# Kernel optimization log

Measured on AMD Instinct MI355X. Metric: run time of the kernel, lower is better.

The kernel has to match this reference:

```python
import jax, jax.numpy as jnp
import numpy as np

NV, NR = 30000, 1000
EVV, EVI, EIV = 400000, 120000, 120000
VD, RD, ED = 16, 8, 2
HID, OUT, H1 = 64, 64, 2


def _seg_softmax(logits, seg, n):
    # numerically stable segment softmax over destination nodes
    m = jax.ops.segment_max(logits, seg, num_segments=n)
    m = jnp.where(jnp.isfinite(m), m, 0.0)
    ex = jnp.exp(logits - m[seg])
    den = jax.ops.segment_sum(ex, seg, num_segments=n)
    return ex / (den[seg] + 1e-16)


def _gatv2(x_src, x_dst, src, dst, ea, Wl, Wr, We, att, b, heads, n_dst, concat):
    # PyG GATv2Conv: e = att . leaky_relu(Wl x_j + Wr x_i + We e_ij); out = sum_j softmax(e) * Wl x_j
    C = att.shape[-1]
    hl = (x_src @ Wl).reshape(-1, heads, C)
    hr = (x_dst @ Wr).reshape(-1, heads, C)
    he = (ea @ We).reshape(-1, heads, C)
    xj = hl[src]                                   # [E, H, C]
    g = jax.nn.leaky_relu(xj + hr[dst] + he, 0.2)
    logits = jnp.einsum('ehc,hc->eh', g, att)      # [E, H]
    alpha = _seg_softmax(logits, dst, n_dst)
    out = jax.ops.segment_sum(xj * alpha[..., None], dst, num_segments=n_dst)
    out = out.reshape(n_dst, heads * C) if concat else out.mean(axis=1)
    return out + b


def _self_loops(src, dst, ea, n):
    # PyG add_self_loops(fill_value='mean'): self-loop edge_attr = per-dst mean of incoming edge_attr
    deg = jax.ops.segment_sum(jnp.ones((ea.shape[0],), ea.dtype), dst, num_segments=n)
    mean = jax.ops.segment_sum(ea, dst, num_segments=n) / jnp.maximum(deg, 1.0)[:, None]
    ar = jnp.arange(n, dtype=src.dtype)
    return jnp.concatenate([src, ar]), jnp.concatenate([dst, ar]), jnp.concatenate([ea, mean], axis=0)


def _ln(x, g, b):
    m = x.mean(-1, keepdims=True)
    v = ((x - m) ** 2).mean(-1, keepdims=True)
    return (x - m) * jax.lax.rsqrt(v + 1e-5) * g + b


def setup_inputs() -> dict:
    key = jax.random.key(0)
    ks = iter(jax.random.split(key, 80))
    def rn(shape, s=1.0):
        return jax.random.normal(next(ks), shape, jnp.float32) * s
    def ri(n, hi):
        return jax.random.randint(next(ks), (n,), 0, hi, jnp.int32)
    d = {'x_veh': rn((NV, VD)), 'x_rsu': rn((NR, RD)),
         'ea_v2v': rn((EVV, ED)), 'ea_v2i': rn((EVI, ED)), 'ea_i2v': rn((EIV, ED)),
         'src_v2v': ri(EVV, NV), 'dst_v2v': ri(EVV, NV),
         'src_v2i': ri(EVI, NV), 'dst_v2i': ri(EVI, NR),
         'src_i2v': ri(EIV, NR), 'dst_i2v': ri(EIV, NV)}
    H1C = H1 * HID
    for rel, di_s, di_d in (('vv', VD, VD), ('vi', VD, RD), ('iv', RD, VD)):
        d['Wl_' + rel + '1'] = rn((di_s, H1C), 0.1)
        d['Wr_' + rel + '1'] = rn((di_d, H1C), 0.1)
        d['We_' + rel + '1'] = rn((ED, H1C), 0.1)
        d['att_' + rel + '1'] = rn((H1, HID), 0.1)
        d['b_' + rel + '1'] = jnp.zeros((H1C,), jnp.float32)
    for rel in ('vv', 'vi', 'iv'):
        d['Wl_' + rel + '2'] = rn((H1C, OUT), 0.1)
        d['Wr_' + rel + '2'] = rn((H1C, OUT), 0.1)
        d['We_' + rel + '2'] = rn((ED, OUT), 0.1)
        d['att_' + rel + '2'] = rn((1, OUT), 0.1)
        d['b_' + rel + '2'] = jnp.zeros((OUT,), jnp.float32)
    d['ln_vg'] = jnp.ones((OUT,), jnp.float32)
    d['ln_vb'] = jnp.zeros((OUT,), jnp.float32)
    d['ln_rg'] = jnp.ones((OUT,), jnp.float32)
    d['ln_rb'] = jnp.zeros((OUT,), jnp.float32)
    return d


def reference(x_veh, x_rsu, ea_v2v, ea_v2i, ea_i2v,
              src_v2v, dst_v2v, src_v2i, dst_v2i, src_i2v, dst_i2v,
              Wl_vv1, Wr_vv1, We_vv1, att_vv1, b_vv1,
              Wl_vi1, Wr_vi1, We_vi1, att_vi1, b_vi1,
              Wl_iv1, Wr_iv1, We_iv1, att_iv1, b_iv1,
              Wl_vv2, Wr_vv2, We_vv2, att_vv2, b_vv2,
              Wl_vi2, Wr_vi2, We_vi2, att_vi2, b_vi2,
              Wl_iv2, Wr_iv2, We_iv2, att_iv2, b_iv2,
              ln_vg, ln_vb, ln_rg, ln_rb):
    s_vv, d_vv, ea_vv = _self_loops(src_v2v, dst_v2v, ea_v2v, NV)
    # layer 1 (heads=2, concat=True), HeteroConv aggr='sum'
    v1 = (_gatv2(x_veh, x_veh, s_vv, d_vv, ea_vv, Wl_vv1, Wr_vv1, We_vv1, att_vv1, b_vv1, H1, NV, True)
          + _gatv2(x_rsu, x_veh, src_i2v, dst_i2v, ea_i2v, Wl_iv1, Wr_iv1, We_iv1, att_iv1, b_iv1, H1, NV, True))
    r1 = _gatv2(x_veh, x_rsu, src_v2i, dst_v2i, ea_v2i, Wl_vi1, Wr_vi1, We_vi1, att_vi1, b_vi1, H1, NR, True)
    v1 = jax.nn.elu(v1)
    r1 = jax.nn.elu(r1)
    # layer 2 (heads=1, concat=False -> mean over 1 head)
    v2 = (_gatv2(v1, v1, s_vv, d_vv, ea_vv, Wl_vv2, Wr_vv2, We_vv2, att_vv2, b_vv2, 1, NV, False)
          + _gatv2(r1, v1, src_i2v, dst_i2v, ea_i2v, Wl_iv2, Wr_iv2, We_iv2, att_iv2, b_iv2, 1, NV, False))
    r2 = _gatv2(v1, r1, src_v2i, dst_v2i, ea_v2i, Wl_vi2, Wr_vi2, We_vi2, att_vi2, b_vi2, 1, NR, False)
    return jnp.concatenate([_ln(v2, ln_vg, ln_vb), _ln(r2, ln_rg, ln_rb)], axis=0)
```

## Files before the change

kernel.cpp:

```cpp
#include <hip/hip_runtime.h>
#include <hip/hip_fp16.h>

constexpr int NV = 30000, NR = 1000;
constexpr int EVV = 400000, EVI = 120000, EIV = 120000;
constexpr int ETOT = EVV + EIV + EVI;
constexpr int VB = (NV + 3) / 4;
constexpr float LOFF = 4.0f;

struct __align__(8) Edge { int s; __half2 ea; };
struct __align__(16) TRec { int s; int d; __half2 ea; int r; };
typedef __half2 h2;

__device__ __forceinline__ h2 h2shfl_xor(h2 v, int m) {
  int i = *(int*)&v;
  i = __shfl_xor(i, m);
  return *(h2*)&i;
}
__device__ __forceinline__ h2 h2max(h2 a, h2 b) {
  h2 r;
  asm("v_pk_max_f16 %0, %1, %2" : "=v"(r) : "v"(a), "v"(b));
  return r;
}

constexpr size_t OFF_CUR_VV = 0;
constexpr size_t OFF_CUR_IV = OFF_CUR_VV + NV;
constexpr size_t OFF_CUR_VI = OFF_CUR_IV + NV;
constexpr size_t ZERO_END   = OFF_CUR_VI + NR;
constexpr size_t OFF_PTR_VV = ZERO_END;
constexpr size_t OFF_PTR_IV = OFF_PTR_VV + NV + 2;
constexpr size_t OFF_PTR_VI = OFF_PTR_IV + NV + 2;
constexpr size_t OFF_E_VV   = (OFF_PTR_VI + NR + 2 + 3) & ~(size_t)3;
constexpr size_t OFF_E_IV   = OFF_E_VV + (size_t)EVV * 2;
constexpr size_t OFF_E_VI   = OFF_E_IV + (size_t)EIV * 2;
constexpr size_t OFF_TMP    = (OFF_E_VI + (size_t)EVI * 2 + 3) & ~(size_t)3;
constexpr size_t OFF_H      = (OFF_TMP + (size_t)ETOT * 4 + 3) & ~(size_t)3;
constexpr size_t OFF_HL_VV1 = OFF_H;
constexpr size_t OFF_HR_VV1 = OFF_HL_VV1 + (size_t)NV * 64;
constexpr size_t OFF_HR_IV1 = OFF_HR_VV1 + (size_t)NV * 64;
constexpr size_t OFF_HL_VI1 = OFF_HR_IV1 + (size_t)NV * 64;
// ... 142 lines not shown
  for (int i = tid; i < ROWS * K / 2; i += 64 * NW) {
    int gi = r0 * (K / 2) + i;
    float2 f = (gi < n * (K / 2)) ? __half22float2(X2[gi]) : make_float2(0.f, 0.f);
    ((float*)xs)[2 * i] = f.x;
    ((float*)xs)[2 * i + 1] = f.y;
  }
  __syncthreads();
  int lane = tid & 63, wv = tid >> 6;
  const float* __restrict__ W = wv == 0 ? W0 : wv == 1 ? W1 : wv == 2 ? W2 : W3;
  __half* __restrict__ Y = wv == 0 ? Y0 : wv == 1 ? Y1 : wv == 2 ? Y2 : Y3;
  float acc[ROWS];
#pragma unroll
  for (int r = 0; r < ROWS; r++) acc[r] = 0.f;
  for (int k4 = 0; k4 < K / 4; k4++) {
    float w0 = W[(4 * k4 + 0) * 64 + lane];
    float w1 = W[(4 * k4 + 1) * 64 + lane];
    float w2 = W[(4 * k4 + 2) * 64 + lane];
    float w3 = W[(4 * k4 + 3) * 64 + lane];
#pragma unroll
    for (int r = 0; r < ROWS; r++) {
      float4 x4 = *(const float4*)&xs[r][4 * k4];
      acc[r] = fmaf(x4.x, w0, acc[r]);
      acc[r] = fmaf(x4.y, w1, acc[r]);
      acc[r] = fmaf(x4.z, w2, acc[r]);
      acc[r] = fmaf(x4.w, w3, acc[r]);
    }
  }
#pragma unroll
  for (int r = 0; r < ROWS; r++)
    if (r0 + r < n) Y[(size_t)(r0 + r) * 64 + lane] = __float2half(acc[r]);
}


template<bool SELF>
__device__ __forceinline__ void gatW2(int d, int lane, int eg, int cg,
    int b, int cnt, int es0, int eab0,
    const Edge* __restrict__ ed,
    const __half* __restrict__ hl, float4 hrr,
    const float* __restrict__ We, const float* __restrict__ att,
    float* acc, float& den0, float& den1) {
  h2 hrc2[4], av2[4], w02[4], w12[4];
  const h2* hrp = (const h2*)&hrr;
#pragma unroll
  for (int j = 0; j < 4; j++) hrc2[j] = hrp[j];
#pragma unroll
  for (int j = 0; j < 4; j++) {
    int c = cg * 4 + j;
    av2[j] = __floats2half2_rn(att[c], att[64 + c]);
    w02[j] = __floats2half2_rn(We[c], We[64 + c]);
    w12[j] = __floats2half2_rn(We[128 + c], We[192 + c]);
  }
  const h2 c02 = __float2half2_rn(0.2f);
  h2 acc2[4];
#pragma unroll
  for (int j = 0; j < 4; j++) acc2[j] = __float2half2_rn(0.f);
  float sum0 = 0.f, sum1 = 0.f;
  auto proc = [&](float4 r, int eab, bool v) {
    const h2* hp = (const h2*)&r;
    h2 eh = *(h2*)&eab;
    h2 ef0 = __low2half2(eh), ef1 = __high2half2(eh);
    h2 lacc = __float2half2_rn(0.f);
#pragma unroll
    for (int j = 0; j < 4; j++) {
      h2 g = __hfma2(ef0, w02[j], __hadd2(hp[j], hrc2[j]));
      g = __hfma2(ef1, w12[j], g);
      h2 lr = h2max(g, __hmul2(c02, g));
      lacc = __hfma2(lr, av2[j], lacc);
    }
#pragma unroll
    for (int o = 1; o <= 8; o <<= 1) lacc = __hadd2(lacc, h2shfl_xor(lacc, o));
    float2 lf = __half22float2(lacc);
    float ex0 = v ? __expf(lf.x - LOFF) : 0.f;
    float ex1 = v ? __expf(lf.y - LOFF) : 0.f;
    h2 exh = __floats2half2_rn(ex0, ex1);
#pragma unroll
    for (int j = 0; j < 4; j++) acc2[j] = __hfma2(exh, hp[j], acc2[j]);
    den0 += ex0; den1 += ex1;
  };
  auto doWin = [&](int es, int eab, int wlen) {
    int kk = 0;
    for (; kk + 16 <= wlen; kk += 16) {
      int k0 = kk + eg, k1 = kk + 4 + eg, k2 = kk + 8 + eg, k3 = kk + 12 + eg;
      int s0 = __shfl(es, k0), ea0 = __shfl(eab, k0);
      int s1 = __shfl(es, k1), ea1 = __shfl(eab, k1);
      int s2 = __shfl(es, k2), ea2 = __shfl(eab, k2);
      int s3 = __shfl(es, k3), ea3 = __shfl(eab, k3);
      float4 r0 = *(const float4*)&hl[(size_t)s0 * 128 + cg * 8];
      float4 r1 = *(const float4*)&hl[(size_t)s1 * 128 + cg * 8];
      float4 r2 = *(const float4*)&hl[(size_t)s2 * 128 + cg * 8];
      float4 r3 = *(const float4*)&hl[(size_t)s3 * 128 + cg * 8];
      proc(r0, ea0, true);
      proc(r1, ea1, true);
      proc(r2, ea2, true);
      proc(r3, ea3, true);
    }
    for (; kk < wlen; kk += 4) {
      int k0 = kk + eg;
      int s0 = __shfl(es, k0), ea0 = __shfl(eab, k0);
      float4 r0 = *(const float4*)&hl[(size_t)s0 * 128 + cg * 8];
      proc(r0, ea0, k0 < wlen);
    }
  };
  if (SELF) {
    float2 f = __half22float2(*(h2*)&eab0);
    sum0 += f.x; sum1 += f.y;
  }
  doWin(es0, eab0, min(64, cnt));
  for (int wf = 64; wf < cnt; wf += 64) {
    int idx = wf + lane;
    int es = 0, eab = 0;
    if (idx < cnt) { Edge e = ed[b + idx]; es = e.s; eab = *(const int*)&e.ea; }
    if (SELF) {
      float2 f = __half22float2(*(h2*)&eab);
      sum0 += f.x; sum1 += f.y;
    }
    doWin(es, eab, min(64, cnt - wf));
  }
  if (SELF) {
#pragma unroll
    for (int o = 1; o <= 32; o <<= 1) { sum0 += __shfl_xor(sum0, o); sum1 += __shfl_xor(sum1, o); }
    float dg = fmaxf((float)cnt, 1.f);
    __half2 mh = __floats2half2_rn(sum0 / dg, sum1 / dg);
    int meab = *(const int*)&mh;
    float4 rS = *(const float4*)&hl[(size_t)d * 128 + cg * 8];
    proc(rS, meab, eg == 0);
  }
#pragma unroll
  for (int o = 16; o <= 32; o <<= 1) {
#pragma unroll
    for (int j = 0; j < 4; j++) acc2[j] = __hadd2(acc2[j], h2shfl_xor(acc2[j], o));
    den0 += __shfl_xor(den0, o);
    den1 += __shfl_xor(den1, o);
  }
#pragma unroll
  for (int j = 0; j < 4; j++) {
    float2 f = __half22float2(acc2[j]);
    acc[2 * j] = f.x; acc[2 * j + 1] = f.y;
  }
}

template<bool SELF>
__device__ __forceinline__ void gatW1(int d, int lane, int eg8, int cg8,
    int b, int cnt, int es0, int eab0,
    const Edge* __restrict__ ed,
    const __half* __restrict__ hl, float4 hrr,
    const float* __restrict__ We, const float* __restrict__ att,
    float* acc, float& den) {
  h2 hrc2[4], av2[4], w02[4], w12[4];
  const h2* hrp = (const h2*)&hrr;
#pragma unroll
  for (int j = 0; j < 4; j++) hrc2[j] = hrp[j];
#pragma unroll
  for (int j = 0; j < 4; j++) {
    int c = cg8 * 8 + 2 * j;
    av2[j] = __floats2half2_rn(att[c], att[c + 1]);
    w02[j] = __floats2half2_rn(We[c], We[c + 1]);
    w12[j] = __floats2half2_rn(We[64 + c], We[64 + c + 1]);
  }
  const h2 c02 = __float2half2_rn(0.2f);
  h2 acc2[4];
#pragma unroll
  for (int j = 0; j < 4; j++) acc2[j] = __float2half2_rn(0.f);
  float sum0 = 0.f, sum1 = 0.f;
  auto proc = [&](float4 r, int eab, bool v) {
    const h2* hp = (const h2*)&r;
    h2 eh = *(h2*)&eab;
    h2 ef0 = __low2half2(eh), ef1 = __high2half2(eh);
    h2 lacc = __float2half2_rn(0.f);
#pragma unroll
    for (int j = 0; j < 4; j++) {
      h2 g = __hfma2(ef0, w02[j], __hadd2(hp[j], hrc2[j]));
      g = __hfma2(ef1, w12[j], g);
      h2 lr = h2max(g, __hmul2(c02, g));
      lacc = __hfma2(lr, av2[j], lacc);
    }
#pragma unroll
    for (int o = 1; o <= 4; o <<= 1) lacc = __hadd2(lacc, h2shfl_xor(lacc, o));
    float2 lf = __half22float2(lacc);
    float ex = v ? __expf(lf.x + lf.y - LOFF) : 0.f;
    h2 exh = __float2half2_rn(ex);
#pragma unroll
    for (int j = 0; j < 4; j++) acc2[j] = __hfma2(exh, hp[j], acc2[j]);
    den += ex;
  };
  auto doWin = [&](int es, int eab, int wlen) {
    int kk = 0;
    for (; kk + 32 <= wlen; kk += 32) {
      int k0 = kk + eg8, k1 = kk + 8 + eg8, k2 = kk + 16 + eg8, k3 = kk + 24 + eg8;
      int s0 = __shfl(es, k0), ea0 = __shfl(eab, k0);
      int s1 = __shfl(es, k1), ea1 = __shfl(eab, k1);
      int s2 = __shfl(es, k2), ea2 = __shfl(eab, k2);
      int s3 = __shfl(es, k3), ea3 = __shfl(eab, k3);
      float4 r0 = *(const float4*)&hl[(size_t)s0 * 64 + cg8 * 8];
      float4 r1 = *(const float4*)&hl[(size_t)s1 * 64 + cg8 * 8];
      float4 r2 = *(const float4*)&hl[(size_t)s2 * 64 + cg8 * 8];
      float4 r3 = *(const float4*)&hl[(size_t)s3 * 64 + cg8 * 8];
      proc(r0, ea0, true);
      proc(r1, ea1, true);
      proc(r2, ea2, true);
      proc(r3, ea3, true);
    }
    for (; kk < wlen; kk += 8) {
      int k0 = kk + eg8;
      int s0 = __shfl(es, k0), ea0 = __shfl(eab, k0);
      float4 r0 = *(const float4*)&hl[(size_t)s0 * 64 + cg8 * 8];
      proc(r0, ea0, k0 < wlen);
    }
  };
  if (SELF) {
    float2 f = __half22float2(*(h2*)&eab0);
    sum0 += f.x; sum1 += f.y;
  }
  doWin(es0, eab0, min(64, cnt));
  for (int wf = 64; wf < cnt; wf += 64) {
    int idx = wf + lane;
    int es = 0, eab = 0;
    if (idx < cnt) { Edge e = ed[b + idx]; es = e.s; eab = *(const int*)&e.ea; }
    if (SELF) {
      float2 f = __half22float2(*(h2*)&eab);
      sum0 += f.x; sum1 += f.y;
    }
    doWin(es, eab, min(64, cnt - wf));
  }
  if (SELF) {
#pragma unroll
    for (int o = 1; o <= 32; o <<= 1) { sum0 += __shfl_xor(sum0, o); sum1 += __shfl_xor(sum1, o); }
    float dg = fmaxf((float)cnt, 1.f);
    __half2 mh = __floats2half2_rn(sum0 / dg, sum1 / dg);
    int meab = *(const int*)&mh;
    float4 rS = *(const float4*)&hl[(size_t)d * 64 + cg8 * 8];
    proc(rS, meab, eg8 == 0);
  }
#pragma unroll
  for (int o = 8; o <= 32; o <<= 1) {
#pragma unroll
    for (int j = 0; j < 4; j++) acc2[j] = __hadd2(acc2[j], h2shfl_xor(acc2[j], o));
    den += __shfl_xor(den, o);
  }
#pragma unroll
  for (int j = 0; j < 4; j++) {
    float2 f = __half22float2(acc2[j]);
    acc[2 * j] = f.x; acc[2 * j + 1] = f.y;
  }
}

__global__ __launch_bounds__(256) void k_gat_l1(
    const int* ptr_vv, const Edge* e_vv,
    const __half* hl_vv, const __half* hr_vv, const float* We_vv, const float* att_vv,
    const int* ptr_iv, const Edge* e_iv,
    const __half* hl_iv, const __half* hr_iv, const float* We_iv, const float* att_iv,
    const int* ptr_vi, const Edge* e_vi,
    const __half* hl_vi, const __half* hr_vi, const float* We_vi, const float* att_vi,
    const float* b_vv, const float* b_iv, const float* b_vi,
    __half* __restrict__ v1, __half* __restrict__ r1) {
  __shared__ float sm[4][16][10];
  int lane = threadIdx.x & 63, wv = threadIdx.x >> 6;
  int eg = lane >> 4, cg = lane & 15;
  if (blockIdx.x >= NR) {
    int w = (blockIdx.x - NR) * 4 + wv;
    if (w >= NV) return;
    int b1 = ptr_vv[w], c1 = ptr_vv[w + 1] - b1;
    int b2 = ptr_iv[w], c2 = ptr_iv[w + 1] - b2;
    int es1 = 0, ea1 = 0, es2 = 0, ea2 = 0;
    if (lane < c1) { Edge e = e_vv[b1 + lane]; es1 = e.s; ea1 = *(const int*)&e.ea; }
    if (lane < c2) { Edge e = e_iv[b2 + lane]; es2 = e.s; ea2 = *(const int*)&e.ea; }
    float4 hrv = *(const float4*)&hr_vv[(size_t)w * 128 + cg * 8];
    float4 hri = *(const float4*)&hr_iv[(size_t)w * 128 + cg * 8];
    float acc[8];
    float d0 = 0.f, d1 = 0.f, oc[8];
    gatW2<true>(w, lane, eg, cg, b1, c1, es1, ea1, e_vv, hl_vv, hrv, We_vv, att_vv, acc, d0, d1);
#pragma unroll
    for (int j = 0; j < 8; j++) oc[j] = acc[j] / (((j & 1) ? d1 : d0) + 1e-16f);
    d0 = d1 = 0.f;
    gatW2<false>(w, lane, eg, cg, b2, c2, es2, ea2, e_iv, hl_iv, hri, We_iv, att_iv, acc, d0, d1);
#pragma unroll
    for (int j = 0; j < 8; j++) oc[j] += acc[j] / (((j & 1) ? d1 : d0) + 1e-16f);
    if (eg == 0) {
      float x[8];
#pragma unroll
      for (int j = 0; j < 8; j++) {
        int c = cg * 4 + (j >> 1);
        int idx = (j & 1) * 64 + c;
        float v = oc[j] + b_vv[idx] + b_iv[idx];
        x[j] = v > 0.f ? v : __expf(v) - 1.f;
      }
      __half2 h0a = __floats2half2_rn(x[0], x[2]), h0b = __floats2half2_rn(x[4], x[6]);
      __half2 h1a = __floats2half2_rn(x[1], x[3]), h1b = __floats2half2_rn(x[5], x[7]);
      float2 p0, p1;
      ((__half2*)&p0)[0] = h0a; ((__half2*)&p0)[1] = h0b;
      ((__half2*)&p1)[0] = h1a; ((__half2*)&p1)[1] = h1b;
      *(float2*)&v1[(size_t)w * 128 + cg * 4]      = p0;
      *(float2*)&v1[(size_t)w * 128 + 64 + cg * 4] = p1;
    }
  } else {
    int dd = blockIdx.x;
    int bfull = ptr_vi[dd], cntf = ptr_vi[dd + 1] - bfull;
    int q = (cntf + 3) >> 2;
    int off = min(wv * q, cntf);
    int cnt = min(q, cntf - off);
    int b = bfull + off;
    int es0 = 0, ea0 = 0;
    if (lane < cnt) { Edge e = e_vi[b + lane]; es0 = e.s; ea0 = *(const int*)&e.ea; }
    float4 hrr = *(const float4*)&hr_vi[(size_t)dd * 128 + cg * 8];
    float acc[8];
    float d0 = 0.f, d1 = 0.f;
    gatW2<false>(dd, lane, eg, cg, b, cnt, es0, ea0, e_vi, hl_vi, hrr, We_vi, att_vi, acc, d0, d1);
    if (eg == 0) {
#pragma unroll
      for (int j = 0; j < 8; j++) sm[wv][cg][j] = acc[j];
      sm[wv][cg][8] = d0; sm[wv][cg][9] = d1;
    }
    __syncthreads();
    if (wv == 0) {
#pragma unroll
      for (int j = 0; j < 8; j++)
        acc[j] = sm[0][cg][j] + sm[1][cg][j] + sm[2][cg][j] + sm[3][cg][j];
      d0 = sm[0][cg][8] + sm[1][cg][8] + sm[2][cg][8] + sm[3][cg][8];
      d1 = sm[0][cg][9] + sm[1][cg][9] + sm[2][cg][9] + sm[3][cg][9];
      if (eg == 0) {
        float x[8];
#pragma unroll
        for (int j = 0; j < 8; j++) {
          int c = cg * 4 + (j >> 1);
          int idx = (j & 1) * 64 + c;
          float v = acc[j] / (((j & 1) ? d1 : d0) + 1e-16f) + b_vi[idx];
          x[j] = v > 0.f ? v : __expf(v) - 1.f;
        }
        __half2 h0a = __floats2half2_rn(x[0], x[2]), h0b = __floats2half2_rn(x[4], x[6]);
        __half2 h1a = __floats2half2_rn(x[1], x[3]), h1b = __floats2half2_rn(x[5], x[7]);
        float2 p0, p1;
        ((__half2*)&p0)[0] = h0a; ((__half2*)&p0)[1] = h0b;
        ((__half2*)&p1)[0] = h1a; ((__half2*)&p1)[1] = h1b;
        *(float2*)&r1[(size_t)dd * 128 + cg * 4]      = p0;
        *(float2*)&r1[(size_t)dd * 128 + 64 + cg * 4] = p1;
      }
    }
  }
}

__global__ __launch_bounds__(256) void k_gat_l2(
    const int* ptr_vv, const Edge* e_vv,
    const __half* hl_vv, const __half* hr_vv, const float* We_vv, const float* att_vv,
    const int* ptr_iv, const Edge* e_iv,
    const __half* hl_iv, const __half* hr_iv, const float* We_iv, const float* att_iv,
    const int* ptr_vi, const Edge* e_vi,
    const __half* hl_vi, const __half* hr_vi, const float* We_vi, const float* att_vi,
    const float* b_vv, const float* b_iv, const float* b_vi,
    const float* ln_vg, const float* ln_vb, const float* ln_rg, const float* ln_rb,
    float* __restrict__ out) {
  __shared__ float sm[4][8][9];
  int lane = threadIdx.x & 63, wv = threadIdx.x >> 6;
  int eg8 = lane >> 3, cg8 = lane & 7;
  if (blockIdx.x >= NR) {
    int w = (blockIdx.x - NR) * 4 + wv;
    if (w >= NV) return;
    int b1 = ptr_vv[w], c1 = ptr_vv[w + 1] - b1;
    int b2 = ptr_iv[w], c2 = ptr_iv[w + 1] - b2;
    int es1 = 0, ea1 = 0, es2 = 0, ea2 = 0;
    if (lane < c1) { Edge e = e_vv[b1 + lane]; es1 = e.s; ea1 = *(const int*)&e.ea; }
    if (lane < c2) { Edge e = e_iv[b2 + lane]; es2 = e.s; ea2 = *(const int*)&e.ea; }
    float4 hrv = *(const float4*)&hr_vv[(size_t)w * 64 + cg8 * 8];
    float4 hri = *(const float4*)&hr_iv[(size_t)w * 64 + cg8 * 8];
    float acc[8];
    float dn = 0.f, oc[8];
    gatW1<true>(w, lane, eg8, cg8, b1, c1, es1, ea1, e_vv, hl_vv, hrv, We_vv, att_vv, acc, dn);
#pragma unroll
    for (int j = 0; j < 8; j++) oc[j] = acc[j] / (dn + 1e-16f);
    dn = 0.f;
    gatW1<false>(w, lane, eg8, cg8, b2, c2, es2, ea2, e_iv, hl_iv, hri, We_iv, att_iv, acc, dn);
    float x[8], s = 0.f;
#pragma unroll
    for (int j = 0; j < 8; j++) {
      int c = cg8 * 8 + j;
      x[j] = oc[j] + acc[j] / (dn + 1e-16f) + b_vv[c] + b_iv[c];
      s += x[j];
    }
#pragma unroll
    for (int o = 1; o <= 4; o <<= 1) s += __shfl_xor(s, o);
    float mu = s * (1.f / 64.f);
    float v = 0.f;
#pragma unroll
    for (int j = 0; j < 8; j++) { float dx = x[j] - mu; v = fmaf(dx, dx, v); }
#pragma unroll
    for (int o = 1; o <= 4; o <<= 1) v += __shfl_xor(v, o);
    float rstd = rsqrtf(v * (1.f / 64.f) + 1e-5f);
    if (eg8 == 0) {
      float4 o0, o1;
      float* ov = (float*)&o0;
#pragma unroll
      for (int j = 0; j < 4; j++) {
        int c = cg8 * 8 + j;
        ov[j] = (x[j] - mu) * rstd * ln_vg[c] + ln_vb[c];
      }
      ov = (float*)&o1;
#pragma unroll
      for (int j = 0; j < 4; j++) {
        int c = cg8 * 8 + 4 + j;
        ov[j] = (x[4 + j] - mu) * rstd * ln_vg[c] + ln_vb[c];
      }
      *(float4*)&out[(size_t)w * 64 + cg8 * 8]     = o0;
      *(float4*)&out[(size_t)w * 64 + cg8 * 8 + 4] = o1;
    }
  } else {
    int dd = blockIdx.x;
    int bfull = ptr_vi[dd], cntf = ptr_vi[dd + 1] - bfull;
    int q = (cntf + 3) >> 2;
    int off = min(wv * q, cntf);
    int cnt = min(q, cntf - off);
    int b = bfull + off;
    int es0 = 0, ea0 = 0;
    if (lane < cnt) { Edge e = e_vi[b + lane]; es0 = e.s; ea0 = *(const int*)&e.ea; }
    float4 hrr = *(const float4*)&hr_vi[(size_t)dd * 64 + cg8 * 8];
    float acc[8];
    float dn = 0.f;
    gatW1<false>(dd, lane, eg8, cg8, b, cnt, es0, ea0, e_vi, hl_vi, hrr, We_vi, att_vi, acc, dn);
    if (eg8 == 0) {
#pragma unroll
      for (int j = 0; j < 8; j++) sm[wv][cg8][j] = acc[j];
      sm[wv][cg8][8] = dn;
    }
    __syncthreads();
    if (wv == 0) {
#pragma unroll
      for (int j = 0; j < 8; j++)
        acc[j] = sm[0][cg8][j] + sm[1][cg8][j] + sm[2][cg8][j] + sm[3][cg8][j];
      dn = sm[0][cg8][8] + sm[1][cg8][8] + sm[2][cg8][8] + sm[3][cg8][8];
      float x[8], s = 0.f;
#pragma unroll
      for (int j = 0; j < 8; j++) {
        int c = cg8 * 8 + j;
        x[j] = acc[j] / (dn + 1e-16f) + b_vi[c];
        s += x[j];
      }
#pragma unroll
      for (int o = 1; o <= 4; o <<= 1) s += __shfl_xor(s, o);
      float mu = s * (1.f / 64.f);
      float v = 0.f;
#pragma unroll
      for (int j = 0; j < 8; j++) { float dx = x[j] - mu; v = fmaf(dx, dx, v); }
#pragma unroll
      for (int o = 1; o <= 4; o <<= 1) v += __shfl_xor(v, o);
      float rstd = rsqrtf(v * (1.f / 64.f) + 1e-5f);
      if (eg8 == 0) {
#pragma unroll
        for (int j = 0; j < 8; j++) {
          int c = cg8 * 8 + j;
          out[(size_t)(NV + dd) * 64 + c] = (x[j] - mu) * rstd * ln_rg[c] + ln_rb[c];
        }
      }
    }
  }
}

extern "C" void kernel_launch(void* const* d_in, const int* in_sizes, int n_in,
                              void* d_out, int out_size, void* d_ws, size_t ws_size,
                              hipStream_t stream) {
  const float* x_veh  = (const float*)d_in[0];
  const float* x_rsu  = (const float*)d_in[1];
  const float* ea_vv  = (const float*)d_in[2];
// ... 53 lines not shown
  Edge* e_iv = (Edge*)(ws + OFF_E_IV);
  Edge* e_vi = (Edge*)(ws + OFF_E_VI);
  TRec* tmp  = (TRec*)(ws + OFF_TMP);

  __half* hl_vv1 = (__half*)(ws + OFF_HL_VV1);
  __half* hr_vv1 = (__half*)(ws + OFF_HR_VV1);
  __half* hr_iv1 = (__half*)(ws + OFF_HR_IV1);
  __half* hl_vi1 = (__half*)(ws + OFF_HL_VI1);
  __half* hl_iv1 = (__half*)(ws + OFF_HL_IV1);
  __half* hr_vi1 = (__half*)(ws + OFF_HR_VI1);
  __half* v1 = (__half*)(ws + OFF_V1);
  __half* r1 = (__half*)(ws + OFF_R1);
  __half* hl_vv2 = (__half*)(ws + OFF_HL_VV2);
  __half* hr_vv2 = (__half*)(ws + OFF_HR_VV2);
  __half* hr_iv2 = (__half*)(ws + OFF_HR_IV2);
  __half* hl_vi2 = (__half*)(ws + OFF_HL_VI2);
  __half* hl_iv2 = (__half*)(ws + OFF_HL_IV2);
  __half* hr_vi2 = (__half*)(ws + OFF_HR_VI2);

  (void)hipMemsetAsync(ws, 0, ZERO_END * sizeof(float), stream);

  k_build1<<<(ETOT + 255) / 256, 256, 0, stream>>>(
      src_vv, dst_vv, ea_vv, src_iv, dst_iv, ea_iv, src_vi, dst_vi, ea_vi,
      cur_vv, cur_iv, cur_vi, tmp);
  k_scan3<<<3, 1024, 0, stream>>>(cur_vv, ptr_vv, NV, cur_iv, ptr_iv, NV, cur_vi, ptr_vi, NR);
  k_build2<<<(ETOT + 255) / 256, 256, 0, stream>>>(tmp, ptr_vv, ptr_iv, ptr_vi,
      e_vv, e_iv, e_vi);

  k_gemm1<16, 4><<<(NV + 7) / 8, 256, 0, stream>>>(x_veh,
      Wl_vv1, Wr_vv1, Wr_iv1, Wl_vi1, hl_vv1, hr_vv1, hr_iv1, hl_vi1, NV);
  k_gemm1<8, 2><<<(NR + 7) / 8, 256, 0, stream>>>(x_rsu,
      Wl_iv1, Wr_vi1, nullptr, nullptr, hl_iv1, hr_vi1, nullptr, nullptr, NR);

  k_gat_l1<<<NR + VB, 256, 0, stream>>>(
      ptr_vv, e_vv, hl_vv1, hr_vv1, We_vv1, att_vv1,
      ptr_iv, e_iv, hl_iv1, hr_iv1, We_iv1, att_iv1,
      ptr_vi, e_vi, hl_vi1, hr_vi1, We_vi1, att_vi1,
      b_vv1, b_iv1, b_vi1, v1, r1);

  k_gemm2<4><<<(NV + 15) / 16, 256, 0, stream>>>(v1,
      Wl_vv2, Wr_vv2, Wr_iv2, Wl_vi2, hl_vv2, hr_vv2, hr_iv2, hl_vi2, NV);
  k_gemm2<2><<<(NR + 15) / 16, 128, 0, stream>>>(r1,
      Wl_iv2, Wr_vi2, nullptr, nullptr, hl_iv2, hr_vi2, nullptr, nullptr, NR);

  k_gat_l2<<<NR + VB, 256, 0, stream>>>(
      ptr_vv, e_vv, hl_vv2, hr_vv2, We_vv2, att_vv2,
      ptr_iv, e_iv, hl_iv2, hr_iv2, We_iv2, att_iv2,
      ptr_vi, e_vi, hl_vi2, hr_vi2, We_vi2, att_vi2,
      b_vv2, b_iv2, b_vi2, ln_vg, ln_vb, ln_rg, ln_rb, out);
  (void)in_sizes; (void)n_in; (void)out_size; (void)ws_size;
}
```

Baseline: 317.6 us.

## Split each vehicle node's edge work across two wavefronts with LDS combine

Each vehicle destination node is now handled by two wavefronts instead of one. One takes the first half of the v2v edges, the other takes the remaining v2v edges plus all i2v edges. Partial numerators, denominators and edge-attribute sums are combined through shared memory after a barrier, and the self-loop term is then applied by the first wavefront. This aims to cut per-node serial latency and balance uneven degrees, at the cost of doubling the vehicle block count, adding a block-wide barrier, and leaving the second wavefront idle during the epilogue.

```diff
diff --git a/kernel.cpp b/kernel.cpp
--- a/kernel.cpp
+++ b/kernel.cpp
@@ -4,7 +4,7 @@
 constexpr int NV = 30000, NR = 1000;
 constexpr int EVV = 400000, EVI = 120000, EIV = 120000;
 constexpr int ETOT = EVV + EIV + EVI;
-constexpr int VB = (NV + 3) / 4;
+constexpr int VB2 = NV / 2;
 constexpr float LOFF = 4.0f;
 
 struct __align__(8) Edge { int s; __half2 ea; };
@@ -213,13 +213,12 @@
 }
 
 
-template<bool SELF>
-__device__ __forceinline__ void gatW2(int d, int lane, int eg, int cg,
+__device__ __forceinline__ void gatP2(int lane, int eg, int cg,
     int b, int cnt, int es0, int eab0,
     const Edge* __restrict__ ed,
     const __half* __restrict__ hl, float4 hrr,
     const float* __restrict__ We, const float* __restrict__ att,
-    float* acc, float& den0, float& den1) {
+    float* acc, float& den0, float& den1, float& sum0, float& sum1) {
   h2 hrc2[4], av2[4], w02[4], w12[4];
   const h2* hrp = (const h2*)&hrr;
 #pragma unroll
@@ -235,7 +234,7 @@
   h2 acc2[4];
 #pragma unroll
   for (int j = 0; j < 4; j++) acc2[j] = __float2half2_rn(0.f);
-  float sum0 = 0.f, sum1 = 0.f;
+  den0 = den1 = 0.f; sum0 = 0.f; sum1 = 0.f;
   auto proc = [&](float4 r, int eab, bool v) {
     const h2* hp = (const h2*)&r;
     h2 eh = *(h2*)&eab;
@@ -282,7 +281,7 @@
       proc(r0, ea0, k0 < wlen);
     }
   };
-  if (SELF) {
+  {
     float2 f = __half22float2(*(h2*)&eab0);
     sum0 += f.x; sum1 += f.y;
   }
@@ -291,20 +290,9 @@
     int idx = wf + lane;
     int es = 0, eab = 0;
     if (idx < cnt) { Edge e = ed[b + idx]; es = e.s; eab = *(const int*)&e.ea; }
-    if (SELF) {
-      float2 f = __half22float2(*(h2*)&eab);
-      sum0 += f.x; sum1 += f.y;
-    }
+    float2 f = __half22float2(*(h2*)&eab);
+    sum0 += f.x; sum1 += f.y;
     doWin(es, eab, min(64, cnt - wf));
-  }
-  if (SELF) {
-#pragma unroll
-    for (int o = 1; o <= 32; o <<= 1) { sum0 += __shfl_xor(sum0, o); sum1 += __shfl_xor(sum1, o); }
-    float dg = fmaxf((float)cnt, 1.f);
-    __half2 mh = __floats2half2_rn(sum0 / dg, sum1 / dg);
-    int meab = *(const int*)&mh;
-    float4 rS = *(const float4*)&hl[(size_t)d * 128 + cg * 8];
-    proc(rS, meab, eg == 0);
   }
 #pragma unroll
   for (int o = 16; o <= 32; o <<= 1) {
@@ -314,19 +302,20 @@
     den1 += __shfl_xor(den1, o);
   }
 #pragma unroll
+  for (int o = 1; o <= 32; o <<= 1) { sum0 += __shfl_xor(sum0, o); sum1 += __shfl_xor(sum1, o); }
+#pragma unroll
   for (int j = 0; j < 4; j++) {
     float2 f = __half22float2(acc2[j]);
     acc[2 * j] = f.x; acc[2 * j + 1] = f.y;
   }
 }
 
-template<bool SELF>
-__device__ __forceinline__ void gatW1(int d, int lane, int eg8, int cg8,
+__device__ __forceinline__ void gatP1(int lane, int eg8, int cg8,
     int b, int cnt, int es0, int eab0,
     const Edge* __restrict__ ed,
     const __half* __restrict__ hl, float4 hrr,
     const float* __restrict__ We, const float* __restrict__ att,
-    float* acc, float& den) {
+    float* acc, float& den, float& sum0, float& sum1) {
   h2 hrc2[4], av2[4], w02[4], w12[4];
   const h2* hrp = (const h2*)&hrr;
 #pragma unroll
@@ -342,7 +331,7 @@
   h2 acc2[4];
 #pragma unroll
   for (int j = 0; j < 4; j++) acc2[j] = __float2half2_rn(0.f);
-  float sum0 = 0.f, sum1 = 0.f;
+  den = 0.f; sum0 = 0.f; sum1 = 0.f;
   auto proc = [&](float4 r, int eab, bool v) {
     const h2* hp = (const h2*)&r;
     h2 eh = *(h2*)&eab;
@@ -388,7 +377,7 @@
       proc(r0, ea0, k0 < wlen);
     }
   };
-  if (SELF) {
+  {
     float2 f = __half22float2(*(h2*)&eab0);
     sum0 += f.x; sum1 += f.y;
   }
@@ -397,20 +386,9 @@
     int idx = wf + lane;
     int es = 0, eab = 0;
     if (idx < cnt) { Edge e = ed[b + idx]; es = e.s; eab = *(const int*)&e.ea; }
-    if (SELF) {
-      float2 f = __half22float2(*(h2*)&eab);
-      sum0 += f.x; sum1 += f.y;
-    }
+    float2 f = __half22float2(*(h2*)&eab);
+    sum0 += f.x; sum1 += f.y;
     doWin(es, eab, min(64, cnt - wf));
-  }
-  if (SELF) {
-#pragma unroll
-    for (int o = 1; o <= 32; o <<= 1) { sum0 += __shfl_xor(sum0, o); sum1 += __shfl_xor(sum1, o); }
-    float dg = fmaxf((float)cnt, 1.f);
-    __half2 mh = __floats2half2_rn(sum0 / dg, sum1 / dg);
-    int meab = *(const int*)&mh;
-    float4 rS = *(const float4*)&hl[(size_t)d * 64 + cg8 * 8];
-    proc(rS, meab, eg8 == 0);
   }
 #pragma unroll
   for (int o = 8; o <= 32; o <<= 1) {
@@ -418,6 +396,8 @@
     for (int j = 0; j < 4; j++) acc2[j] = __hadd2(acc2[j], h2shfl_xor(acc2[j], o));
     den += __shfl_xor(den, o);
   }
+#pragma unroll
+  for (int o = 1; o <= 32; o <<= 1) { sum0 += __shfl_xor(sum0, o); sum1 += __shfl_xor(sum1, o); }
 #pragma unroll
   for (int j = 0; j < 4; j++) {
     float2 f = __half22float2(acc2[j]);
@@ -434,44 +414,117 @@
     const __half* hl_vi, const __half* hr_vi, const float* We_vi, const float* att_vi,
     const float* b_vv, const float* b_iv, const float* b_vi,
     __half* __restrict__ v1, __half* __restrict__ r1) {
-  __shared__ float sm[4][16][10];
+  __shared__ float smA[4][16][12];
+  __shared__ float smB[2][16][10];
   int lane = threadIdx.x & 63, wv = threadIdx.x >> 6;
   int eg = lane >> 4, cg = lane & 15;
   if (blockIdx.x >= NR) {
-    int w = (blockIdx.x - NR) * 4 + wv;
-    if (w >= NV) return;
+    int role = wv & 1;
+    int w = (blockIdx.x - NR) * 2 + (wv >> 1);
     int b1 = ptr_vv[w], c1 = ptr_vv[w + 1] - b1;
     int b2 = ptr_iv[w], c2 = ptr_iv[w + 1] - b2;
-    int es1 = 0, ea1 = 0, es2 = 0, ea2 = 0;
-    if (lane < c1) { Edge e = e_vv[b1 + lane]; es1 = e.s; ea1 = *(const int*)&e.ea; }
-    if (lane < c2) { Edge e = e_iv[b2 + lane]; es2 = e.s; ea2 = *(const int*)&e.ea; }
+    int hsplit = min(c1, (c1 + c2 + 1) >> 1);
     float4 hrv = *(const float4*)&hr_vv[(size_t)w * 128 + cg * 8];
-    float4 hri = *(const float4*)&hr_iv[(size_t)w * 128 + cg * 8];
-    float acc[8];
-    float d0 = 0.f, d1 = 0.f, oc[8];
-    gatW2<true>(w, lane, eg, cg, b1, c1, es1, ea1, e_vv, hl_vv, hrv, We_vv, att_vv, acc, d0, d1);
-#pragma unroll
-    for (int j = 0; j < 8; j++) oc[j] = acc[j] / (((j & 1) ? d1 : d0) + 1e-16f);
-    d0 = d1 = 0.f;
-    gatW2<false>(w, lane, eg, cg, b2, c2, es2, ea2, e_iv, hl_iv, hri, We_iv, att_iv, acc, d0, d1);
-#pragma unroll
-    for (int j = 0; j < 8; j++) oc[j] += acc[j] / (((j & 1) ? d1 : d0) + 1e-16f);
-    if (eg == 0) {
-      float x[8];
-#pragma unroll
-      for (int j = 0; j < 8; j++) {
-        int c = cg * 4 + (j >> 1);
-        int idx = (j & 1) * 64 + c;
-        float v = oc[j] + b_vv[idx] + b_iv[idx];
-        x[j] = v > 0.f ? v : __expf(v) - 1.f;
-      }
-      __half2 h0a = __floats2half2_rn(x[0], x[2]), h0b = __floats2half2_rn(x[4], x[6]);
-      __half2 h1a = __floats2half2_rn(x[1], x[3]), h1b = __floats2half2_rn(x[5], x[7]);
-      float2 p0, p1;
-      ((__half2*)&p0)[0] = h0a; ((__half2*)&p0)[1] = h0b;
-      ((__half2*)&p1)[0] = h1a; ((__half2*)&p1)[1] = h1b;
-      *(float2*)&v1[(size_t)w * 128 + cg * 4]      = p0;
-      *(float2*)&v1[(size_t)w * 128 + 64 + cg * 4] = p1;
+    float acc[8], d0, d1, s0, s1;
+    if (role == 0) {
+      int es0 = 0, ea0 = 0;
+      if (lane < hsplit) { Edge e = e_vv[b1 + lane]; es0 = e.s; ea0 = *(const int*)&e.ea; }
+      gatP2(lane, eg, cg, b1, hsplit, es0, ea0, e_vv, hl_vv, hrv, We_vv, att_vv, acc, d0, d1, s0, s1);
+      if (eg == 0) {
+#pragma unroll
+        for (int j = 0; j < 8; j++) smA[wv][cg][j] = acc[j];
+        smA[wv][cg][8] = d0; smA[wv][cg][9] = d1;
+        smA[wv][cg][10] = s0; smA[wv][cg][11] = s1;
+      }
+    } else {
+      int bB = b1 + hsplit, cB = c1 - hsplit;
+      int es1 = 0, ea1 = 0, es2 = 0, ea2 = 0;
+      if (lane < cB) { Edge e = e_vv[bB + lane]; es1 = e.s; ea1 = *(const int*)&e.ea; }
+      if (lane < c2) { Edge e = e_iv[b2 + lane]; es2 = e.s; ea2 = *(const int*)&e.ea; }
+      gatP2(lane, eg, cg, bB, cB, es1, ea1, e_vv, hl_vv, hrv, We_vv, att_vv, acc, d0, d1, s0, s1);
+      if (eg == 0) {
+#pragma unroll
+        for (int j = 0; j < 8; j++) smA[wv][cg][j] = acc[j];
+        smA[wv][cg][8] = d0; smA[wv][cg][9] = d1;
+        smA[wv][cg][10] = s0; smA[wv][cg][11] = s1;
+      }
+      float4 hri = *(const float4*)&hr_iv[(size_t)w * 128 + cg * 8];
+      float si0, si1;
+      gatP2(lane, eg, cg, b2, c2, es2, ea2, e_iv, hl_iv, hri, We_iv, att_iv, acc, d0, d1, si0, si1);
+      if (eg == 0) {
+#pragma unroll
+        for (int j = 0; j < 8; j++) smB[wv >> 1][cg][j] = acc[j];
+        smB[wv >> 1][cg][8] = d0; smB[wv >> 1][cg][9] = d1;
+      }
+    }
+    __syncthreads();
+    if (role == 0) {
+      float accI[8], di0, di1;
+#pragma unroll
+      for (int j = 0; j < 8; j++) acc[j] = smA[wv][cg][j] + smA[wv + 1][cg][j];
+      d0 = smA[wv][cg][8] + smA[wv + 1][cg][8];
+      d1 = smA[wv][cg][9] + smA[wv + 1][cg][9];
+      s0 = smA[wv][cg][10] + smA[wv + 1][cg][10];
+      s1 = smA[wv][cg][11] + smA[wv + 1][cg][11];
+#pragma unroll
+      for (int j = 0; j < 8; j++) accI[j] = smB[wv >> 1][cg][j];
+      di0 = smB[wv >> 1][cg][8]; di1 = smB[wv >> 1][cg][9];
+      float dg = fmaxf((float)c1, 1.f);
+      h2 meh = __floats2half2_rn(s0 / dg, s1 / dg);
+      h2 hrc2[4], av2[4], w02[4], w12[4];
+      const h2* hrp = (const h2*)&hrv;
+#pragma unroll
+      for (int j = 0; j < 4; j++) hrc2[j] = hrp[j];
+#pragma unroll
+      for (int j = 0; j < 4; j++) {
+        int c = cg * 4 + j;
+        av2[j] = __floats2half2_rn(att_vv[c], att_vv[64 + c]);
+        w02[j] = __floats2half2_rn(We_vv[c], We_vv[64 + c]);
+        w12[j] = __floats2half2_rn(We_vv[128 + c], We_vv[192 + c]);
+      }
+      const h2 c02 = __float2half2_rn(0.2f);
+      float4 rS = *(const float4*)&hl_vv[(size_t)w * 128 + cg * 8];
+      const h2* hp = (const h2*)&rS;
+      h2 ef0 = __low2half2(meh), ef1 = __high2half2(meh);
+      h2 lacc = __float2half2_rn(0.f);
+#pragma unroll
+      for (int j = 0; j < 4; j++) {
+        h2 g = __hfma2(ef0, w02[j], __hadd2(hp[j], hrc2[j]));
+        g = __hfma2(ef1, w12[j], g);
+        h2 lr = h2max(g, __hmul2(c02, g));
+        lacc = __hfma2(lr, av2[j], lacc);
+      }
+#pragma unroll
+      for (int o = 1; o <= 8; o <<= 1) lacc = __hadd2(lacc, h2shfl_xor(lacc, o));
+      float2 lf = __half22float2(lacc);
+      float ex0 = (eg == 0) ? __expf(lf.x - LOFF) : 0.f;
+      float ex1 = (eg == 0) ? __expf(lf.y - LOFF) : 0.f;
+#pragma unroll
+      for (int j = 0; j < 4; j++) {
+        float2 f = __half22float2(hp[j]);
+        acc[2 * j]     += ex0 * f.x;
+        acc[2 * j + 1] += ex1 * f.y;
+      }
+      d0 += ex0; d1 += ex1;
+      if (eg == 0) {
+        float x[8];
+#pragma unroll
+        for (int j = 0; j < 8; j++) {
+          int c = cg * 4 + (j >> 1);
+          int idx = (j & 1) * 64 + c;
+          float dv = (j & 1) ? d1 : d0;
+          float dvi = (j & 1) ? di1 : di0;
+          float v = acc[j] / (dv + 1e-16f) + accI[j] / (dvi + 1e-16f) + b_vv[idx] + b_iv[idx];
+          x[j] = v > 0.f ? v : __expf(v) - 1.f;
+        }
+        __half2 h0a = __floats2half2_rn(x[0], x[2]), h0b = __floats2half2_rn(x[4], x[6]);
+        __half2 h1a = __floats2half2_rn(x[1], x[3]), h1b = __floats2half2_rn(x[5], x[7]);
+        float2 p0, p1;
+        ((__half2*)&p0)[0] = h0a; ((__half2*)&p0)[1] = h0b;
+        ((__half2*)&p1)[0] = h1a; ((__half2*)&p1)[1] = h1b;
+        *(float2*)&v1[(size_t)w * 128 + cg * 4]      = p0;
+        *(float2*)&v1[(size_t)w * 128 + 64 + cg * 4] = p1;
+      }
     }
   } else {
     int dd = blockIdx.x;
@@ -483,38 +536,35 @@
     int es0 = 0, ea0 = 0;
     if (lane < cnt) { Edge e = e_vi[b + lane]; es0 = e.s; ea0 = *(const int*)&e.ea; }
     float4 hrr = *(const float4*)&hr_vi[(size_t)dd * 128 + cg * 8];
-    float acc[8];
-    float d0 = 0.f, d1 = 0.f;
-    gatW2<false>(dd, lane, eg, cg, b, cnt, es0, ea0, e_vi, hl_vi, hrr, We_vi, att_vi, acc, d0, d1);
+    float acc[8], d0, d1, s0, s1;
+    gatP2(lane, eg, cg, b, cnt, es0, ea0, e_vi, hl_vi, hrr, We_vi, att_vi, acc, d0, d1, s0, s1);
     if (eg == 0) {
 #pragma unroll
-      for (int j = 0; j < 8; j++) sm[wv][cg][j] = acc[j];
-      sm[wv][cg][8] = d0; sm[wv][cg][9] = d1;
+      for (int j = 0; j < 8; j++) smA[wv][cg][j] = acc[j];
+      smA[wv][cg][8] = d0; smA[wv][cg][9] = d1;
     }
     __syncthreads();
-    if (wv == 0) {
+    if (wv == 0 && eg == 0) {
 #pragma unroll
       for (int j = 0; j < 8; j++)
-        acc[j] = sm[0][cg][j] + sm[1][cg][j] + sm[2][cg][j] + sm[3][cg][j];
-      d0 = sm[0][cg][8] + sm[1][cg][8] + sm[2][cg][8] + sm[3][cg][8];
-      d1 = sm[0][cg][9] + sm[1][cg][9] + sm[2][cg][9] + sm[3][cg][9];
-      if (eg == 0) {
-        float x[8];
-#pragma unroll
-        for (int j = 0; j < 8; j++) {
-          int c = cg * 4 + (j >> 1);
-          int idx = (j & 1) * 64 + c;
-          float v = acc[j] / (((j & 1) ? d1 : d0) + 1e-16f) + b_vi[idx];
-          x[j] = v > 0.f ? v : __expf(v) - 1.f;
-        }
-        __half2 h0a = __floats2half2_rn(x[0], x[2]), h0b = __floats2half2_rn(x[4], x[6]);
-        __half2 h1a = __floats2half2_rn(x[1], x[3]), h1b = __floats2half2_rn(x[5], x[7]);
-        float2 p0, p1;
-        ((__half2*)&p0)[0] = h0a; ((__half2*)&p0)[1] = h0b;
-        ((__half2*)&p1)[0] = h1a; ((__half2*)&p1)[1] = h1b;
-        *(float2*)&r1[(size_t)dd * 128 + cg * 4]      = p0;
-        *(float2*)&r1[(size_t)dd * 128 + 64 + cg * 4] = p1;
-      }
+        acc[j] = smA[0][cg][j] + smA[1][cg][j] + smA[2][cg][j] + smA[3][cg][j];
+      d0 = smA[0][cg][8] + smA[1][cg][8] + smA[2][cg][8] + smA[3][cg][8];
+      d1 = smA[0][cg][9] + smA[1][cg][9] + smA[2][cg][9] + smA[3][cg][9];
+      float x[8];
+#pragma unroll
+      for (int j = 0; j < 8; j++) {
+        int c = cg * 4 + (j >> 1);
+        int idx = (j & 1) * 64 + c;
+        float v = acc[j] / (((j & 1) ? d1 : d0) + 1e-16f) + b_vi[idx];
+        x[j] = v > 0.f ? v : __expf(v) - 1.f;
+      }
+      __half2 h0a = __floats2half2_rn(x[0], x[2]), h0b = __floats2half2_rn(x[4], x[6]);
+      __half2 h1a = __floats2half2_rn(x[1], x[3]), h1b = __floats2half2_rn(x[5], x[7]);
+      float2 p0, p1;
+      ((__half2*)&p0)[0] = h0a; ((__half2*)&p0)[1] = h0b;
+      ((__half2*)&p1)[0] = h1a; ((__half2*)&p1)[1] = h1b;
+      *(float2*)&r1[(size_t)dd * 128 + cg * 4]      = p0;
+      *(float2*)&r1[(size_t)dd * 128 + 64 + cg * 4] = p1;
     }
   }
 }
@@ -529,58 +579,127 @@
     const float* b_vv, const float* b_iv, const float* b_vi,
     const float* ln_vg, const float* ln_vb, const float* ln_rg, const float* ln_rb,
     float* __restrict__ out) {
-  __shared__ float sm[4][8][9];
+  __shared__ float smA[4][8][11];
+  __shared__ float smB[2][8][9];
   int lane = threadIdx.x & 63, wv = threadIdx.x >> 6;
   int eg8 = lane >> 3, cg8 = lane & 7;
   if (blockIdx.x >= NR) {
-    int w = (blockIdx.x - NR) * 4 + wv;
-    if (w >= NV) return;
+    int role = wv & 1;
+    int w = (blockIdx.x - NR) * 2 + (wv >> 1);
     int b1 = ptr_vv[w], c1 = ptr_vv[w + 1] - b1;
     int b2 = ptr_iv[w], c2 = ptr_iv[w + 1] - b2;
-    int es1 = 0, ea1 = 0, es2 = 0, ea2 = 0;
-    if (lane < c1) { Edge e = e_vv[b1 + lane]; es1 = e.s; ea1 = *(const int*)&e.ea; }
-    if (lane < c2) { Edge e = e_iv[b2 + lane]; es2 = e.s; ea2 = *(const int*)&e.ea; }
+    int hsplit = min(c1, (c1 + c2 + 1) >> 1);
     float4 hrv = *(const float4*)&hr_vv[(size_t)w * 64 + cg8 * 8];
-    float4 hri = *(const float4*)&hr_iv[(size_t)w * 64 + cg8 * 8];
-    float acc[8];
-    float dn = 0.f, oc[8];
-    gatW1<true>(w, lane, eg8, cg8, b1, c1, es1, ea1, e_vv, hl_vv, hrv, We_vv, att_vv, acc, dn);
-#pragma unroll
-    for (int j = 0; j < 8; j++) oc[j] = acc[j] / (dn + 1e-16f);
-    dn = 0.f;
-    gatW1<false>(w, lane, eg8, cg8, b2, c2, es2, ea2, e_iv, hl_iv, hri, We_iv, att_iv, acc, dn);
-    float x[8], s = 0.f;
-#pragma unroll
-    for (int j = 0; j < 8; j++) {
-      int c = cg8 * 8 + j;
-      x[j] = oc[j] + acc[j] / (dn + 1e-16f) + b_vv[c] + b_iv[c];
-      s += x[j];
-    }
-#pragma unroll
-    for (int o = 1; o <= 4; o <<= 1) s += __shfl_xor(s, o);
-    float mu = s * (1.f / 64.f);
-    float v = 0.f;
-#pragma unroll
-    for (int j = 0; j < 8; j++) { float dx = x[j] - mu; v = fmaf(dx, dx, v); }
-#pragma unroll
-    for (int o = 1; o <= 4; o <<= 1) v += __shfl_xor(v, o);
-    float rstd = rsqrtf(v * (1.f / 64.f) + 1e-5f);
-    if (eg8 == 0) {
-      float4 o0, o1;
-      float* ov = (float*)&o0;
+    float acc[8], dn, s0, s1;
+    if (role == 0) {
+      int es0 = 0, ea0 = 0;
+      if (lane < hsplit) { Edge e = e_vv[b1 + lane]; es0 = e.s; ea0 = *(const int*)&e.ea; }
+      gatP1(lane, eg8, cg8, b1, hsplit, es0, ea0, e_vv, hl_vv, hrv, We_vv, att_vv, acc, dn, s0, s1);
+      if (eg8 == 0) {
+#pragma unroll
+        for (int j = 0; j < 8; j++) smA[wv][cg8][j] = acc[j];
+        smA[wv][cg8][8] = dn; smA[wv][cg8][9] = s0; smA[wv][cg8][10] = s1;
+      }
+    } else {
+      int bB = b1 + hsplit, cB = c1 - hsplit;
+      int es1 = 0, ea1 = 0, es2 = 0, ea2 = 0;
+      if (lane < cB) { Edge e = e_vv[bB + lane]; es1 = e.s; ea1 = *(const int*)&e.ea; }
+      if (lane < c2) { Edge e = e_iv[b2 + lane]; es2 = e.s; ea2 = *(const int*)&e.ea; }
+      gatP1(lane, eg8, cg8, bB, cB, es1, ea1, e_vv, hl_vv, hrv, We_vv, att_vv, acc, dn, s0, s1);
+      if (eg8 == 0) {
+#pragma unroll
+        for (int j = 0; j < 8; j++) smA[wv][cg8][j] = acc[j];
+        smA[wv][cg8][8] = dn; smA[wv][cg8][9] = s0; smA[wv][cg8][10] = s1;
+      }
+      float4 hri = *(const float4*)&hr_iv[(size_t)w * 64 + cg8 * 8];
+      float si0, si1;
+      gatP1(lane, eg8, cg8, b2, c2, es2, ea2, e_iv, hl_iv, hri, We_iv, att_iv, acc, dn, si0, si1);
+      if (eg8 == 0) {
+#pragma unroll
+        for (int j = 0; j < 8; j++) smB[wv >> 1][cg8][j] = acc[j];
+        smB[wv >> 1][cg8][8] = dn;
+      }
+    }
+    __syncthreads();
+    if (role == 0) {
+      float accI[8], dni;
+#pragma unroll
+      for (int j = 0; j < 8; j++) acc[j] = smA[wv][cg8][j] + smA[wv + 1][cg8][j];
+      dn = smA[wv][cg8][8] + smA[wv + 1][cg8][8];
+      s0 = smA[wv][cg8][9] + smA[wv + 1][cg8][9];
+      s1 = smA[wv][cg8][10] + smA[wv + 1][cg8][10];
+#pragma unroll
+      for (int j = 0; j < 8; j++) accI[j] = smB[wv >> 1][cg8][j];
+      dni = smB[wv >> 1][cg8][8];
+      float dg = fmaxf((float)c1, 1.f);
+      h2 meh = __floats2half2_rn(s0 / dg, s1 / dg);
+      h2 hrc2[4], av2[4], w02[4], w12[4];
+      const h2* hrp = (const h2*)&hrv;
+#pragma unroll
+      for (int j = 0; j < 4; j++) hrc2[j] = hrp[j];
 #pragma unroll
       for (int j = 0; j < 4; j++) {
+        int c = cg8 * 8 + 2 * j;
+        av2[j] = __floats2half2_rn(att_vv[c], att_vv[c + 1]);
+        w02[j] = __floats2half2_rn(We_vv[c], We_vv[c + 1]);
+        w12[j] = __floats2half2_rn(We_vv[64 + c], We_vv[64 + c + 1]);
+      }
+      const h2 c02 = __float2half2_rn(0.2f);
+      float4 rS = *(const float4*)&hl_vv[(size_t)w * 64 + cg8 * 8];
+      const h2* hp = (const h2*)&rS;
+      h2 ef0 = __low2half2(meh), ef1 = __high2half2(meh);
+      h2 lacc = __float2half2_rn(0.f);
+#pragma unroll
+      for (int j = 0; j < 4; j++) {
+        h2 g = __hfma2(ef0, w02[j], __hadd2(hp[j], hrc2[j]));
+        g = __hfma2(ef1, w12[j], g);
+        h2 lr = h2max(g, __hmul2(c02, g));
+        lacc = __hfma2(lr, av2[j], lacc);
+      }
+#pragma unroll
+      for (int o = 1; o <= 4; o <<= 1) lacc = __hadd2(lacc, h2shfl_xor(lacc, o));
+      float2 lf = __half22float2(lacc);
+      float ex = (eg8 == 0) ? __expf(lf.x + lf.y - LOFF) : 0.f;
+#pragma unroll
+      for (int j = 0; j < 4; j++) {
+        float2 f = __half22float2(hp[j]);
+        acc[2 * j]     += ex * f.x;
+        acc[2 * j + 1] += ex * f.y;
+      }
+      dn += ex;
+      float x[8], s = 0.f;
+#pragma unroll
+      for (int j = 0; j < 8; j++) {
         int c = cg8 * 8 + j;
-        ov[j] = (x[j] - mu) * rstd * ln_vg[c] + ln_vb[c];
-      }
-      ov = (float*)&o1;
-#pragma unroll
-      for (int j = 0; j < 4; j++) {
-        int c = cg8 * 8 + 4 + j;
-        ov[j] = (x[4 + j] - mu) * rstd * ln_vg[c] + ln_vb[c];
-      }
-      *(float4*)&out[(size_t)w * 64 + cg8 * 8]     = o0;
-      *(float4*)&out[(size_t)w * 64 + cg8 * 8 + 4] = o1;
+        x[j] = acc[j] / (dn + 1e-16f) + accI[j] / (dni + 1e-16f) + b_vv[c] + b_iv[c];
+        s += x[j];
+      }
+#pragma unroll
+      for (int o = 1; o <= 4; o <<= 1) s += __shfl_xor(s, o);
+      float mu = s * (1.f / 64.f);
+      float v = 0.f;
+#pragma unroll
+      for (int j = 0; j < 8; j++) { float dx = x[j] - mu; v = fmaf(dx, dx, v); }
+#pragma unroll
+      for (int o = 1; o <= 4; o <<= 1) v += __shfl_xor(v, o);
+      float rstd = rsqrtf(v * (1.f / 64.f) + 1e-5f);
+      if (eg8 == 0) {
+        float4 o0, o1;
+        float* ov = (float*)&o0;
+#pragma unroll
+        for (int j = 0; j < 4; j++) {
+          int c = cg8 * 8 + j;
+          ov[j] = (x[j] - mu) * rstd * ln_vg[c] + ln_vb[c];
+        }
+        ov = (float*)&o1;
+#pragma unroll
+        for (int j = 0; j < 4; j++) {
+          int c = cg8 * 8 + 4 + j;
+          ov[j] = (x[4 + j] - mu) * rstd * ln_vg[c] + ln_vb[c];
+        }
+        *(float4*)&out[(size_t)w * 64 + cg8 * 8]     = o0;
+        *(float4*)&out[(size_t)w * 64 + cg8 * 8 + 4] = o1;
+      }
     }
   } else {
     int dd = blockIdx.x;
@@ -592,20 +711,19 @@
     int es0 = 0, ea0 = 0;
     if (lane < cnt) { Edge e = e_vi[b + lane]; es0 = e.s; ea0 = *(const int*)&e.ea; }
     float4 hrr = *(const float4*)&hr_vi[(size_t)dd * 64 + cg8 * 8];
-    float acc[8];
-    float dn = 0.f;
-    gatW1<false>(dd, lane, eg8, cg8, b, cnt, es0, ea0, e_vi, hl_vi, hrr, We_vi, att_vi, acc, dn);
+    float acc[8], dn, s0, s1;
+    gatP1(lane, eg8, cg8, b, cnt, es0, ea0, e_vi, hl_vi, hrr, We_vi, att_vi, acc, dn, s0, s1);
     if (eg8 == 0) {
 #pragma unroll
-      for (int j = 0; j < 8; j++) sm[wv][cg8][j] = acc[j];
-      sm[wv][cg8][8] = dn;
+      for (int j = 0; j < 8; j++) smA[wv][cg8][j] = acc[j];
+      smA[wv][cg8][8] = dn;
     }
     __syncthreads();
     if (wv == 0) {
 #pragma unroll
       for (int j = 0; j < 8; j++)
-        acc[j] = sm[0][cg8][j] + sm[1][cg8][j] + sm[2][cg8][j] + sm[3][cg8][j];
-      dn = sm[0][cg8][8] + sm[1][cg8][8] + sm[2][cg8][8] + sm[3][cg8][8];
+        acc[j] = smA[0][cg8][j] + smA[1][cg8][j] + smA[2][cg8][j] + smA[3][cg8][j];
+      dn = smA[0][cg8][8] + smA[1][cg8][8] + smA[2][cg8][8] + smA[3][cg8][8];
       float x[8], s = 0.f;
 #pragma unroll
       for (int j = 0; j < 8; j++) {
@@ -725,7 +843,7 @@
   k_gemm1<8, 2><<<(NR + 7) / 8, 256, 0, stream>>>(x_rsu,
       Wl_iv1, Wr_vi1, nullptr, nullptr, hl_iv1, hr_vi1, nullptr, nullptr, NR);
 
-  k_gat_l1<<<NR + VB, 256, 0, stream>>>(
+  k_gat_l1<<<NR + VB2, 256, 0, stream>>>(
       ptr_vv, e_vv, hl_vv1, hr_vv1, We_vv1, att_vv1,
       ptr_iv, e_iv, hl_iv1, hr_iv1, We_iv1, att_iv1,
       ptr_vi, e_vi, hl_vi1, hr_vi1, We_vi1, att_vi1,
@@ -736,7 +854,7 @@
   k_gemm2<2><<<(NR + 15) / 16, 128, 0, stream>>>(r1,
       Wl_iv2, Wr_vi2, nullptr, nullptr, hl_iv2, hr_vi2, nullptr, nullptr, NR);
 
-  k_gat_l2<<<NR + VB, 256, 0, stream>>>(
+  k_gat_l2<<<NR + VB2, 256, 0, stream>>>(
       ptr_vv, e_vv, hl_vv2, hr_vv2, We_vv2, att_vv2,
       ptr_iv, e_iv, hl_iv2, hr_iv2, We_iv2, att_iv2,
       ptr_vi, e_vi, hl_vi2, hr_vi2, We_vi2, att_vi2,
```

New measurement: 375.3 us. 1.18x slower.
